# Performance work log

Measured on AMD Instinct MI355X. Metric: run time of the kernel, lower is better.

## Reference

```python
import jax, jax.numpy as jnp
import numpy as np

EMB_DIM = 4096
N_HEADS = 32
QKV_DIM = EMB_DIM // N_HEADS  # 128
B, S = 4, 4096


def setup_inputs() -> dict:
    key = jax.random.key(0)
    ks = jax.random.split(key, 7)
    std = 1.0 / np.sqrt(EMB_DIM)  # lecun-normal-ish init for DenseGeneral kernels
    x = jax.random.normal(ks[0], (B, S, EMB_DIM), dtype=jnp.float32)
    Wq = jax.random.normal(ks[1], (EMB_DIM, QKV_DIM, N_HEADS), dtype=jnp.float32) * std
    bq = jnp.zeros((QKV_DIM, N_HEADS), dtype=jnp.float32)
    Wk = jax.random.normal(ks[2], (EMB_DIM, QKV_DIM, 1), dtype=jnp.float32) * std
    bk = jnp.zeros((QKV_DIM, 1), dtype=jnp.float32)
    Wv = jax.random.normal(ks[3], (EMB_DIM, QKV_DIM, 1), dtype=jnp.float32) * std
    bv = jnp.zeros((QKV_DIM, 1), dtype=jnp.float32)
    return {"x": x, "Wq": Wq, "bq": bq, "Wk": Wk, "bk": bk, "Wv": Wv, "bv": bv}


def reference(x, Wq, bq, Wk, bk, Wv, bv):
    # q: (B, S, d, h) ; k, v: (B, S, d) -- single shared head (squeeze the 1-axis)
    q = jnp.einsum('bsD,Ddh->bsdh', x, Wq) + bq
    k = (jnp.einsum('bsD,Ddh->bsdh', x, Wk) + bk)[..., 0]
    v = (jnp.einsum('bsD,Ddh->bsdh', x, Wv) + bv)[..., 0]
    qkv_dim = q.shape[-2]
    n_heads = q.shape[-1]
    scale = 1.0 / jnp.sqrt(jnp.asarray(qkv_dim, dtype=q.dtype))
    # Original: scores = q @ swapaxes(repeat(k), -1, -2) -> contracts the HEADS
    # axis per token. With k repeated across heads this equals
    # (sum_h q[..., d, h]) * k[..., e]. einsum sums h (absent from output).
    scores = jnp.einsum('bsdh,bse->bsde', q, k) * scale  # (B, S, d, d)
    p = jax.nn.softmax(scores, axis=-1)
    # out[..., d, h] = sum_e p[..., d, e] * v_rep[..., e, h]; v identical per h.
    o = jnp.einsum('bsde,bse->bsd', p, v)  # (B, S, d)
    out = jnp.broadcast_to(o[..., None], o.shape + (n_heads,))  # (B, S, d, h)
    return out.reshape(x.shape[:-1] + (qkv_dim * n_heads,))
```

## Files before the change

### kernel.cpp

```cpp
#include <hip/hip_runtime.h>

#define EMB  4096
#define DH   128
#define NH   32
#define NTOK 16384
#define NCOL 384

#define BM 64
#define BK 64

typedef __attribute__((ext_vector_type(8))) short short8;
typedef __attribute__((ext_vector_type(4))) short short4_t;
typedef __attribute__((ext_vector_type(4))) float f32x4;

static __device__ __forceinline__ unsigned int cvt2(float a, float b) {
    unsigned int r;
    asm volatile("v_cvt_pk_bf16_f32 %0, %1, %2" : "=v"(r) : "v"(a), "v"(b));
    return r;
}
static __device__ __forceinline__ unsigned short f2bf(float f) {
    unsigned int u = __builtin_bit_cast(unsigned int, f);
    u += 0x7fffu + ((u >> 16) & 1u);
    return (unsigned short)(u >> 16);
}
static __device__ __forceinline__ float exp2_hw(float x) {
#if __has_builtin(__builtin_amdgcn_exp2f)
    return __builtin_amdgcn_exp2f(x);
#else
    float r;
    asm volatile("v_exp_f32 %0, %1\n\ts_nop 1" : "=v"(r) : "v"(x));
    return r;
#endif
}

__global__ void prep_w(const float* __restrict__ Wq, const float* __restrict__ bq,
                       const float* __restrict__ Wk, const float* __restrict__ bk,
                       const float* __restrict__ Wv, const float* __restrict__ bv,
                       unsigned short* __restrict__ W3F, float* __restrict__ bias) {
    const int tid = blockIdx.x * 256 + threadIdx.x;
    const int n  = tid >> 9;
    const int ck = tid & 511;
    const int D0 = ck * 8;

    float v[8];
    if (n < DH) {
#pragma unroll
        for (int e = 0; e < 8; ++e) {
            const float4* p = (const float4*)(Wq + (size_t)(D0 + e) * (DH * NH) + n * NH);
            float s = 0.f;
#pragma unroll
            for (int i = 0; i < 8; ++i) { float4 q = p[i]; s += (q.x + q.y) + (q.z + q.w); }
            v[e] = s;
        }
    } else if (n < 2 * DH) {
#pragma unroll
        for (int e = 0; e < 8; ++e) v[e] = Wk[(size_t)(D0 + e) * DH + (n - DH)];
    } else {
#pragma unroll
        for (int e = 0; e < 8; ++e) v[e] = Wv[(size_t)(D0 + e) * DH + (n - 2 * DH)];
    }

    union { short8 s; unsigned int u[4]; } pk;
#pragma unroll
    for (int j = 0; j < 4; ++j)
        pk.u[j] = (unsigned int)f2bf(v[2 * j]) | ((unsigned int)f2bf(v[2 * j + 1]) << 16);

    const int p    = n >> 6, r = n & 63;
    const int jfr  = r >> 4, lmod = r & 15;
    const int kt   = ck >> 3;
    const int kh   = (ck >> 2) & 1;
    const int lgrp = ck & 3;
    const int lane = lgrp * 16 + lmod;
    char* dst = (char*)W3F + (size_t)p * 524288 + (size_t)kt * 8192
              + (kh * 4 + jfr) * 1024 + lane * 16;
    *(short8*)dst = pk.s;

    if (ck == 0) {
        float b;
        if (n < DH) {
            float s = 0.f;
#pragma unroll
            for (int h = 0; h < NH; ++h) s += bq[n * NH + h];
            b = s;
        } else if (n < 2 * DH) {
            b = bk[n - DH];
        } else {
            b = bv[n - 2 * DH];
        }
        bias[n] = b;
    }
}

__global__ __launch_bounds__(512) void fused_mqa(const float* __restrict__ X,
                         const unsigned short* __restrict__ W3F,
                         const float* __restrict__ bias,
                         float* __restrict__ out) {
    __shared__ __align__(16) unsigned short Asm[BM * BK];
    __shared__ float qsm[32 * NCOL];

    const int bid  = blockIdx.x;
    const int wkid = (bid & 7) * 32 + (bid >> 3);
    const int m0   = wkid * BM;
    const int nt   = EMB / BK;

    const int t = threadIdx.x, lane = t & 63, w = t >> 6;
    const int lmod = lane & 15, lgrp = lane >> 4;

    f32x4 acc[4][3] = {};

    const int arow = w * 8 + (lane >> 3);
    const float* xp = X + (size_t)(m0 + arow) * EMB + (lane & 7) * 4;
    const int ac0 = (lane & 7) >> 1;
    const int ah4 = ((lane & 7) & 1) * 4;

    const char* bp[3];
#pragma unroll
    for (int j = 0; j < 3; ++j) {
        const int f = w * 3 + j;
        bp[j] = (const char*)W3F + (size_t)(f >> 2) * 524288 + (f & 3) * 1024 + lane * 16;
    }

    f32x4 avA[2], avB[2];
    short8 bfA[6], bfB[6];

#define LOAD_AV(T, AV) do { \
    const int tc_ = (T) < nt ? (T) : nt - 1; \
    AV[0] = __builtin_nontemporal_load((const f32x4*)(xp + tc_ * BK)); \
    AV[1] = __builtin_nontemporal_load((const f32x4*)(xp + tc_ * BK + 32)); \
} while (0)

#define LOAD_BF(T, BF) do { \
    const int tc_ = (T) < nt ? (T) : nt - 1; \
    _Pragma("unroll") \
    for (int j = 0; j < 3; ++j) { \
        BF[j]     = *(const short8*)(bp[j] + (size_t)tc_ * 8192); \
        BF[3 + j] = *(const short8*)(bp[j] + (size_t)tc_ * 8192 + 4096); \
    } \
} while (0)

#define WRITE_A(AV) do { \
    union { short4_t s; unsigned int u[2]; } p0, p1; \
    p0.u[0] = cvt2(AV[0].x, AV[0].y);  p0.u[1] = cvt2(AV[0].z, AV[0].w); \
    p1.u[0] = cvt2(AV[1].x, AV[1].y);  p1.u[1] = cvt2(AV[1].z, AV[1].w); \
    *(short4_t*)(&Asm[arow * BK + ((ac0 ^ (arow & 7)) << 3) + ah4]) = p0.s; \
    *(short4_t*)(&Asm[arow * BK + (((ac0 + 4) ^ (arow & 7)) << 3) + ah4]) = p1.s; \
} while (0)

#define COMPUTE(BF) do { \
    _Pragma("unroll") \
    for (int kh = 0; kh < 2; ++kh) { \
        const int cs = ((kh * 4 + lgrp) ^ (lmod & 7)) * 8; \
        short8 af[4]; \
        _Pragma("unroll") \
        for (int i = 0; i < 4; ++i) \
            af[i] = *(const short8*)(&Asm[(i * 16 + lmod) * BK + cs]); \
        _Pragma("unroll") \
        for (int i = 0; i < 4; ++i) \
            _Pragma("unroll") \
            for (int j = 0; j < 3; ++j) \
                acc[i][j] = __builtin_amdgcn_mfma_f32_16x16x32_bf16(af[i], BF[kh * 3 + j], acc[i][j], 0, 0, 0); \
    } \
} while (0)

#define ABAR()  do { asm volatile("s_barrier" ::: "memory"); } while (0)
#define WBAR()  do { asm volatile("s_waitcnt lgkmcnt(0)\n\ts_barrier" ::: "memory"); } while (0)

    LOAD_AV(0, avA);
    LOAD_AV(1, avB);
    LOAD_BF(0, bfA);

    for (int tt = 0; tt < nt; tt += 2) {
        ABAR();
        WRITE_A(avA);
        WBAR();
        LOAD_BF(tt + 1, bfB);
        LOAD_AV(tt + 2, avA);
        COMPUTE(bfA);
        ABAR();
        WRITE_A(avB);
        WBAR();
        LOAD_BF(tt + 2, bfA);
        LOAD_AV(tt + 3, avB);
        COMPUTE(bfB);
    }

    const float c = 0.088388347648318447f * 1.4426950408889634f;
#pragma unroll
    for (int pass = 0; pass < 2; ++pass) {
        __syncthreads();
#pragma unroll
        for (int j = 0; j < 3; ++j) {
            const int col = w * 48 + j * 16 + lmod;
            const float bj = bias[col];
#pragma unroll
            for (int i2 = 0; i2 < 2; ++i2) {
                const int row = i2 * 16 + (lgrp << 2);
#pragma unroll
                for (int r = 0; r < 4; ++r)
                    qsm[(row + r) * NCOL + col] = acc[pass * 2 + i2][j][r] + bj;
            }
        }
        __syncthreads();

        for (int tok = w; tok < 32; tok += 8) {
            const float* row = &qsm[tok * NCOL];
            const float q0  = row[lane],       q1  = row[64 + lane];
            const float kk0 = row[128 + lane], kk1 = row[192 + lane];

            float lmax = fmaxf(kk0, kk1), lmin = fminf(kk0, kk1);
#pragma unroll
            for (int off = 32; off; off >>= 1) {
                lmax = fmaxf(lmax, __shfl_xor(lmax, off));
                lmin = fminf(lmin, __shfl_xor(lmin, off));
            }

            const float a0 = q0 * c, a1 = q1 * c;
            const float m0v = (a0 >= 0.f) ? a0 * lmax : a0 * lmin;
            const float m1v = (a1 >= 0.f) ? a1 * lmax : a1 * lmin;

            float s00 = 0.f, s01 = 0.f, s10 = 0.f, s11 = 0.f;
#pragma unroll 8
            for (int e = 0; e < DH; ++e) {
                const float kv = row[128 + e];
                const float vv = row[256 + e];
                const float p0 = exp2_hw(fmaf(a0, kv, -m0v));
                const float p1 = exp2_hw(fmaf(a1, kv, -m1v));
                s00 += p0;  s01 = fmaf(p0, vv, s01);
                s10 += p1;  s11 = fmaf(p1, vv, s11);
            }
            const float o0 = s01 / s00;
            const float o1 = s11 / s10;

            float* orow = out + (size_t)(m0 + pass * 32 + tok) * (DH * NH);
#pragma unroll
            for (int it = 0; it < 16; ++it) {
                const int idx = it * 64 + lane;
                const int src = (it & 7) * 8 + (lane >> 3);
                const float val = (it < 8) ? __shfl(o0, src) : __shfl(o1, src);
                f32x4 f4 = {val, val, val, val};
                __builtin_nontemporal_store(f4, (f32x4*)(orow + idx * 4));
            }
        }
    }
#undef LOAD_AV
#undef LOAD_BF
#undef WRITE_A
#undef COMPUTE
#undef ABAR
#undef WBAR
}

extern "C" void kernel_launch(void* const* d_in, const int* in_sizes, int n_in,
                              void* d_out, int out_size, void* d_ws, size_t ws_size,
                              hipStream_t stream) {
    const float* x  = (const float*)d_in[0];
    const float* Wq = (const float*)d_in[1];
    const float* bq = (const float*)d_in[2];
    const float* Wk = (const float*)d_in[3];
    const float* bk = (const float*)d_in[4];
    const float* Wv = (const float*)d_in[5];
    const float* bv = (const float*)d_in[6];
    float* out = (float*)d_out;

    char* ws = (char*)d_ws;
    unsigned short* W3F = (unsigned short*)ws;
    float* bias = (float*)(ws + 3145728);

    prep_w<<<(NCOL * 512) / 256, 256, 0, stream>>>(Wq, bq, Wk, bk, Wv, bv, W3F, bias);
    fused_mqa<<<NTOK / BM, 512, 0, stream>>>(x, W3F, bias, out);
}
```

Measured before the change: 160.5 us.

## Double-buffer A tile in LDS with four-deep X prefetch and MFMA priority

Splits the A shared-memory tile into two buffers, so the next tile's bf16 write overlaps the current tile's MFMA compute and each k-step needs one barrier instead of two. X loads are prefetched four tiles ahead using four register sets, hiding global latency longer. Compute sections raise wave priority with s_setprio. The cost is more LDS and more VGPRs, which may lower occupancy or cause spills under the 512-thread launch bound.

```diff
diff --git a/kernel.cpp b/kernel.cpp
--- a/kernel.cpp
+++ b/kernel.cpp
@@ -95,7 +95,7 @@
                          const unsigned short* __restrict__ W3F,
                          const float* __restrict__ bias,
                          float* __restrict__ out) {
-    __shared__ __align__(16) unsigned short Asm[BM * BK];
+    __shared__ __align__(16) unsigned short Asm[2][BM * BK];
     __shared__ float qsm[32 * NCOL];
 
     const int bid  = blockIdx.x;
@@ -120,7 +120,7 @@
         bp[j] = (const char*)W3F + (size_t)(f >> 2) * 524288 + (f & 3) * 1024 + lane * 16;
     }
 
-    f32x4 avA[2], avB[2];
+    f32x4 avA[2], avB[2], avC[2], avD[2];
     short8 bfA[6], bfB[6];
 
 #define LOAD_AV(T, AV) do { \
@@ -138,50 +138,52 @@
     } \
 } while (0)
 
-#define WRITE_A(AV) do { \
+#define WRITE_A(AV, BUF) do { \
     union { short4_t s; unsigned int u[2]; } p0, p1; \
     p0.u[0] = cvt2(AV[0].x, AV[0].y);  p0.u[1] = cvt2(AV[0].z, AV[0].w); \
     p1.u[0] = cvt2(AV[1].x, AV[1].y);  p1.u[1] = cvt2(AV[1].z, AV[1].w); \
-    *(short4_t*)(&Asm[arow * BK + ((ac0 ^ (arow & 7)) << 3) + ah4]) = p0.s; \
-    *(short4_t*)(&Asm[arow * BK + (((ac0 + 4) ^ (arow & 7)) << 3) + ah4]) = p1.s; \
-} while (0)
-
-#define COMPUTE(BF) do { \
+    *(short4_t*)(&(BUF)[arow * BK + ((ac0 ^ (arow & 7)) << 3) + ah4]) = p0.s; \
+    *(short4_t*)(&(BUF)[arow * BK + (((ac0 + 4) ^ (arow & 7)) << 3) + ah4]) = p1.s; \
+} while (0)
+
+#define COMPUTE(AB, BF) do { \
+    __builtin_amdgcn_s_setprio(1); \
     _Pragma("unroll") \
     for (int kh = 0; kh < 2; ++kh) { \
         const int cs = ((kh * 4 + lgrp) ^ (lmod & 7)) * 8; \
         short8 af[4]; \
         _Pragma("unroll") \
         for (int i = 0; i < 4; ++i) \
-            af[i] = *(const short8*)(&Asm[(i * 16 + lmod) * BK + cs]); \
+            af[i] = *(const short8*)(&(AB)[(i * 16 + lmod) * BK + cs]); \
         _Pragma("unroll") \
         for (int i = 0; i < 4; ++i) \
             _Pragma("unroll") \
             for (int j = 0; j < 3; ++j) \
                 acc[i][j] = __builtin_amdgcn_mfma_f32_16x16x32_bf16(af[i], BF[kh * 3 + j], acc[i][j], 0, 0, 0); \
     } \
-} while (0)
-
-#define ABAR()  do { asm volatile("s_barrier" ::: "memory"); } while (0)
-#define WBAR()  do { asm volatile("s_waitcnt lgkmcnt(0)\n\ts_barrier" ::: "memory"); } while (0)
+    __builtin_amdgcn_s_setprio(0); \
+} while (0)
+
+#define IBAR()  do { asm volatile("s_waitcnt lgkmcnt(0)\n\ts_barrier" ::: "memory"); } while (0)
 
     LOAD_AV(0, avA);
-    LOAD_AV(1, avB);
     LOAD_BF(0, bfA);
-
-    for (int tt = 0; tt < nt; tt += 2) {
-        ABAR();
-        WRITE_A(avA);
-        WBAR();
-        LOAD_BF(tt + 1, bfB);
-        LOAD_AV(tt + 2, avA);
-        COMPUTE(bfA);
-        ABAR();
-        WRITE_A(avB);
-        WBAR();
-        LOAD_BF(tt + 2, bfA);
-        LOAD_AV(tt + 3, avB);
-        COMPUTE(bfB);
+    WRITE_A(avA, Asm[0]);
+    LOAD_AV(1, avA);
+    LOAD_AV(2, avB);
+    LOAD_AV(3, avC);
+    LOAD_AV(4, avD);
+    IBAR();
+
+    for (int tt = 0; tt < nt; tt += 4) {
+        WRITE_A(avA, Asm[1]);  LOAD_BF(tt + 1, bfB);  LOAD_AV(tt + 5, avA);
+        COMPUTE(Asm[0], bfA);  IBAR();
+        WRITE_A(avB, Asm[0]);  LOAD_BF(tt + 2, bfA);  LOAD_AV(tt + 6, avB);
+        COMPUTE(Asm[1], bfB);  IBAR();
+        WRITE_A(avC, Asm[1]);  LOAD_BF(tt + 3, bfB);  LOAD_AV(tt + 7, avC);
+        COMPUTE(Asm[0], bfA);  IBAR();
+        WRITE_A(avD, Asm[0]);  LOAD_BF(tt + 4, bfA);  LOAD_AV(tt + 8, avD);
+        COMPUTE(Asm[1], bfB);  IBAR();
     }
 
     const float c = 0.088388347648318447f * 1.4426950408889634f;
@@ -246,8 +248,7 @@
 #undef LOAD_BF
 #undef WRITE_A
 #undef COMPUTE
-#undef ABAR
-#undef WBAR
+#undef IBAR
 }
 
 extern "C" void kernel_launch(void* const* d_in, const int* in_sizes, int n_in,
```

Result: no change. 162.9 us (+1.5%).
